# Optimization experiments

Measured on AMD Instinct MI355X. Metric: run time of the kernel, lower is better.

Reference implementation:

```python
import jax, jax.numpy as jnp
import numpy as np

N, NB, H, D = 192, 3, 8, 10
HU, HE = [16, 8], [4, 2]
Ne = N * N


def setup_inputs() -> dict:
    key = jax.random.key(0)
    ks = jax.random.split(key, 20)
    g = lambda i, s: jax.random.normal(ks[i], s, jnp.float32)
    xav = lambda i, s: g(i, s) * 0.1  # small-scale init standing in for xavier
    return {
        "X": g(0, (N, D)),
        "A": g(1, (NB, N, N)),
        "E": g(2, (NB, N, N)),
        "e2n_adj": g(3, (N, Ne)),
        # node-path params, stacked over [attr, head]
        "w_n0": xav(4, (NB, H, D, HU[0])), "b_n0": jnp.zeros((NB, H, HU[0])),
        "as0": xav(5, (NB, H, HU[0])), "an0": xav(6, (NB, H, HU[0])),
        "w_n1": xav(7, (NB, H, H * HU[0], HU[1])), "b_n1": jnp.zeros((NB, H, HU[1])),
        "as1": xav(8, (NB, H, HU[1])), "an1": xav(9, (NB, H, HU[1])),
        # edge-to-node params, stacked over [head] (shared across attrs)
        "w_e0": xav(10, (H, NB, HE[0])), "b_e0": jnp.zeros((H, HE[0])),
        "w_ct0": xav(11, (H, HU[0] + HE[0], HU[0])), "b_ct0": jnp.zeros((H, HU[0])),
        "aes0": xav(12, (H, HU[0])), "aen0": xav(13, (H, HE[0])),
        "w_e1": xav(14, (H, H * HE[0], HE[1])), "b_e1": jnp.zeros((H, HE[1])),
        "w_ct1": xav(15, (H, HU[1] + HE[1], HU[1])), "b_ct1": jnp.zeros((H, HU[1])),
        "aes1": xav(16, (H, HU[1])), "aen1": xav(17, (H, HE[1])),
    }


def reference(X, A, E, e2n_adj,
              w_n0, b_n0, as0, an0, w_n1, b_n1, as1, an1,
              w_e0, b_e0, w_ct0, b_ct0, aes0, aen0,
              w_e1, b_e1, w_ct1, b_ct1, aes1, aen1):
    # Eval mode: dropout is identity.
    lrelu = lambda x: jax.nn.leaky_relu(x, 0.2)
    nb = A.shape[0]
    n = X.shape[0]
    E_e2n = E.reshape(nb, -1).T  # [Ne, nb]; col attr == E[attr].flatten()
    node_p = [(w_n0, b_n0, as0, an0), (w_n1, b_n1, as1, an1)]
    edge_p = [(w_e0, b_e0, w_ct0, b_ct0, aes0, aen0),
              (w_e1, b_e1, w_ct1, b_ct1, aes1, aen1)]
    outs = []
    for attr in range(nb):
        A_attr = A[attr]
        h_list = [X]
        X_head, X_edge, E_info = X, E_e2n, E[attr]
        for hid in range(len(node_p)):
            wn, bn, asf, anf = (p[attr] for p in node_p[hid])
            we, be, wct, bct, aes, aen = edge_p[hid]
            feats = jnp.einsum('nd,hdf->hnf', X_head, wn)        # [H,N,F]
            fe = jnp.einsum('ed,hdf->hef', X_edge, we)           # [H,Ne,Fe]
            s = jnp.einsum('hnf,hf->hn', feats, aes)
            t = jnp.einsum('hef,hf->he', fe, aen)
            # edge-to-node attention: [H,N,Ne]
            att = jax.nn.softmax(lrelu(s[:, :, None] + t[:, None, :]) + e2n_adj[None], -1)
            nfe = jnp.einsum('hne,hef->hnf', att, fe) + be[:, None, :]
            f2 = jnp.einsum('hnd,hdf->hnf', jnp.concatenate([feats, nfe], -1), wct) + bct[:, None, :]
            s2 = jnp.einsum('hnf,hf->hn', f2, asf)
            t2 = jnp.einsum('hnf,hf->hn', f2, anf)
            d2 = jnp.einsum('hnm,mk->hnk', s2[:, :, None] + t2[:, None, :], E_info)
            att2 = jax.nn.softmax(lrelu(d2) + A_attr[None], -1)  # [H,N,N]
            nf = jax.nn.elu(jnp.einsum('hnm,hmf->hnf', att2, f2) + bn[:, None, :])
            h1 = jnp.transpose(nf, (1, 0, 2)).reshape(n, -1)     # head concat
            h_list.append(h1)
            X_head = h1
            X_edge = jnp.transpose(fe, (1, 0, 2)).reshape(fe.shape[1], -1)
            E_info = att2[-1]  # last head's post-softmax dense (as in torch)
        outs.append(jnp.concatenate(h_list, -1)[:, None, :])  # skip connection
    return jnp.concatenate(outs, 1)  # [N, nb_attribute, D + H*HU0 + H*HU1]
```

## Files before the change

kernel.cpp:

```cpp
#include <hip/hip_runtime.h>
#include <hip/hip_bf16.h>

#define NN 192
#define NBA 3
#define NH 8
#define ND 10
#define NE_ (NN*NN)
#define NE2 (NE_/2)
#define OUTC 202

typedef unsigned int u32;
typedef unsigned short u16;
typedef __attribute__((ext_vector_type(2))) _Float16 h2v;
typedef __attribute__((ext_vector_type(8))) _Float16 f16x8;
typedef __attribute__((ext_vector_type(4))) float f32x4;

static const size_t OFF_ET0P  = 0;
static const size_t OFF_ET50P = OFF_ET0P  + 147456;
static const size_t OFF_ET1P  = OFF_ET50P + 147456;
static const size_t OFF_ET51P = OFF_ET1P  + 147456;
static const size_t OFF_FT0P  = OFF_ET51P + 147456;
static const size_t OFF_FT1P  = OFF_FT0P  + 589824;
static const size_t OFF_EAP   = OFF_FT1P  + 294912;
static const size_t OFF_XH1   = OFF_EAP   + 3538944;
static const size_t OFF_EINF  = OFF_XH1   + 73728;
static const size_t OFF_ES0   = OFF_EINF  + 110592;
static const size_t OFF_ES50  = OFF_ES0   + 4608;
static const size_t OFF_ES1   = OFF_ES50  + 4608;
static const size_t OFF_ES51  = OFF_ES1   + 4608;
static const size_t OFF_WT1   = OFF_ES51  + 4608;
static const size_t OFF_PART  = OFF_WT1   + 3072;
static const size_t OFF_RED   = OFF_PART  + 1474560;
static const size_t OFF_F2    = OFF_RED   + 23040;
static const size_t OFF_S2    = OFF_F2    + 73728;
static const size_t OFF_T2    = OFF_S2    + 4608;
static const size_t OFF_TE    = OFF_T2    + 4608;
static const size_t OFF_CS    = OFF_TE    + 4608;

__device__ __forceinline__ u32 h2u(h2v h) { union { h2v h; u32 u; } c; c.h = h; return c.u; }
__device__ __forceinline__ h2v u2h(u32 u) { union { u32 u; h2v h; } c; c.u = u; return c.h; }
__device__ __forceinline__ u32 packh(float a, float b) {
    h2v h; h.x = (_Float16)a; h.y = (_Float16)b; return h2u(h);
}

__global__ __launch_bounds__(256) void k_pre(
    const float* __restrict__ E, const float* __restrict__ adj,
    const float* __restrict__ X,
    const float* __restrict__ we0, const float* __restrict__ aen0,
    const float* __restrict__ we1, const float* __restrict__ aen1,
    const float* __restrict__ wn0, const float* __restrict__ aes0,
    const float* __restrict__ wn1, const float* __restrict__ aes1,
    u32* __restrict__ et0P, u32* __restrict__ et50P,
    u32* __restrict__ et1P, u32* __restrict__ et51P,
    u32* __restrict__ ft0P, u32* __restrict__ ft1P,
    u32* __restrict__ eaP,
    u32* __restrict__ es0, u32* __restrict__ es50,
    float* __restrict__ wt1)
{
    int b = blockIdx.x, tid = threadIdx.x;
    if (b < 72) {
        __shared__ float w0s[96], a0s[32], w1s[512], a1s[16];
        for (int i = tid; i < 96;  i += 256) w0s[i] = we0[i];
        for (int i = tid; i < 32;  i += 256) a0s[i] = aen0[i];
        for (int i = tid; i < 512; i += 256) w1s[i] = we1[i];
        for (int i = tid; i < 16;  i += 256) a1s[i] = aen1[i];
        __syncthreads();
        int ep = b*256 + tid;
        int e0 = 2*ep;
        float2 E0 = *(const float2*)(E + e0);
        float2 E1 = *(const float2*)(E + NE_ + e0);
        float2 E2 = *(const float2*)(E + 2*NE_ + e0);
        float fa[32], fb[32];
        #pragma unroll
        for (int h = 0; h < 8; h++) {
            float ta = 0.f, tb = 0.f;
            #pragma unroll
            for (int f = 0; f < 4; f++) {
                float wa = w0s[h*12+f], wb = w0s[h*12+4+f], wc = w0s[h*12+8+f];
                float va = E0.x*wa + E1.x*wb + E2.x*wc;
                float vb = E0.y*wa + E1.y*wb + E2.y*wc;
                fa[h*4+f] = va; fb[h*4+f] = vb;
                ft0P[(size_t)(h*4+f)*NE2 + ep] = packh(va, vb);
                ta += va * a0s[h*4+f];
                tb += vb * a0s[h*4+f];
            }
            et0P [h*NE2 + ep] = packh(__expf(ta), __expf(tb));
            et50P[h*NE2 + ep] = packh(__expf(0.2f*ta), __expf(0.2f*tb));
        }
        #pragma unroll
        for (int h = 0; h < 8; h++) {
            float aa = 0.f, ba = 0.f, ab = 0.f, bb = 0.f;
            #pragma unroll
            for (int d = 0; d < 32; d++) {
                float w0 = w1s[(h*32+d)*2], w1 = w1s[(h*32+d)*2+1];
                aa += fa[d] * w0;  ba += fa[d] * w1;
                ab += fb[d] * w0;  bb += fb[d] * w1;
            }
            ft1P[(size_t)(h*2+0)*NE2 + ep] = packh(aa, ab);
            ft1P[(size_t)(h*2+1)*NE2 + ep] = packh(ba, bb);
            float ta = aa*a1s[h*2] + ba*a1s[h*2+1];
            float tb = ab*a1s[h*2] + bb*a1s[h*2+1];
            et1P [h*NE2 + ep] = packh(__expf(ta), __expf(tb));
            et51P[h*NE2 + ep] = packh(__expf(0.2f*ta), __expf(0.2f*tb));
        }
    } else if (b < 1800) {
        int idx = (b - 72)*256 + tid;
        int n = idx / 2304, c8 = idx % 2304;
        const float* ap = adj + (size_t)n*NE_ + c8*16;
        u32 o[8];
        #pragma unroll
        for (int q = 0; q < 4; q++) {
            float4 v = *(const float4*)(ap + q*4);
            o[2*q]   = packh(__expf(v.x), __expf(v.y));
            o[2*q+1] = packh(__expf(v.z), __expf(v.w));
        }
        u32* dst = eaP + (size_t)n*NE2 + c8*8;
        *(uint4*)(dst)     = make_uint4(o[0], o[1], o[2], o[3]);
        *(uint4*)(dst + 4) = make_uint4(o[4], o[5], o[6], o[7]);
    } else if (b == 1800) {
        for (int v = tid; v < 3072; v += 256) {
            int a = v >> 10, rem = v & 1023, h = rem >> 7, d = rem & 127;
            float w = 0.f;
            #pragma unroll
            for (int f = 0; f < 8; f++)
                w += wn1[(((size_t)a*NH + h)*128 + d)*8 + f] * aes1[h*8 + f];
            wt1[v] = w;
        }
    } else {
        int ah = b - 1801;
        int a = ah / NH, h = ah % NH;
        __shared__ float wt0[ND];
        if (tid < ND) {
            float w = 0.f;
            #pragma unroll
            for (int f = 0; f < 16; f++)
                w += wn0[(((size_t)a*NH + h)*ND + tid)*16 + f] * aes0[h*16 + f];
            wt0[tid] = w;
        }
        __syncthreads();
        if (tid < NN) {
            float s = 0.f;
            #pragma unroll
            for (int d = 0; d < ND; d++) s += X[tid*ND + d] * wt0[d];
            es0 [ah*NN + tid] = packh(__expf(s), __expf(s));
            es50[ah*NN + tid] = packh(__expf(0.2f*s), __expf(0.2f*s));
        }
    }
}

template<int FE>
__global__ __launch_bounds__(512, 3) void k_att3(
    const u32* __restrict__ es_,
    const u32* __restrict__ es5_,
    const u32* __restrict__ etP,
    const u32* __restrict__ et5P,
    const u32* __restrict__ feP,
    const u32* __restrict__ eaP,
    float* __restrict__ part)
{
    constexpr int S = 64, EPB = NE_/S, TILES = EPB/32;
    constexpr int EP2 = EPB/2;
    constexpr int ROWP = EP2 + 4;
    constexpr size_t PA = (size_t)S*12*NH*(FE+1)*16;
    __shared__ u32 sea[16*ROWP];

    int h = threadIdx.x >> 6, lane = threadIdx.x & 63;
    int fr = lane & 15, kg = lane >> 4;
    int split = blockIdx.x, ntile = blockIdx.y;
    int nm = ntile*16 + fr;
    int p0 = split*EP2;

    {
        int r = threadIdx.x >> 5, c0 = threadIdx.x & 31;
        const u32* src = eaP + (size_t)(ntile*16 + r)*NE2 + p0;
        #pragma unroll
        for (int i = 0; i < 9; i++)
            sea[r*ROWP + c0 + i*32] = src[c0 + i*32];
    }

    h2v esh[NBA], es5h[NBA];
    #pragma unroll
    for (int a = 0; a < NBA; a++) {
        esh[a]  = u2h(es_ [(a*NH + h)*NN + nm]);
        es5h[a] = u2h(es5_[(a*NH + h)*NN + nm]);
    }

    const u32* etp  = etP  + (size_t)h*NE2 + p0 + kg*4;
    const u32* et5p = et5P + (size_t)h*NE2 + p0 + kg*4;
    const u32* fp   = feP  + ((size_t)h*FE + (fr < FE ? fr : 0))*NE2 + p0 + kg*4;
    u32 bfill = (fr == FE) ? 0x3C003C00u : 0u;
    uint4 bc = make_uint4(bfill, bfill, bfill, bfill);

    f32x4 acc[NBA];
    #pragma unroll
    for (int a = 0; a < NBA; a++) acc[a] = (f32x4){0.f, 0.f, 0.f, 0.f};

    __syncthreads();

    const u32* seap = sea + fr*ROWP + kg*4;
    #pragma unroll 2
    for (int t = 0; t < TILES; t++) {
        uint4 etq  = *(const uint4*)(etp  + t*16);
        uint4 et5q = *(const uint4*)(et5p + t*16);
        uint4 eaq  = *(const uint4*)(seap + t*16);
        uint4 bq = bc;
        if (fr < FE) bq = *(const uint4*)(fp + t*16);
        union { uint4 u; f16x8 v; } B; B.u = bq;

        u32 etw[4]  = {etq.x,  etq.y,  etq.z,  etq.w};
        u32 et5w[4] = {et5q.x, et5q.y, et5q.z, et5q.w};
        u32 eaw[4]  = {eaq.x,  eaq.y,  eaq.z,  eaq.w};
        h2v g1[4], g2[4];
        #pragma unroll
        for (int p = 0; p < 4; p++) {
            h2v ea = u2h(eaw[p]);
            g1[p] = u2h(etw[p])  * ea;
            g2[p] = u2h(et5w[p]) * ea;
        }
        #pragma unroll
        for (int a = 0; a < NBA; a++) {
            union { uint4 u; f16x8 v; } A;
            u32 aw[4];
            #pragma unroll
            for (int p = 0; p < 4; p++) {
                h2v wv = __builtin_elementwise_max(esh[a] * g1[p], es5h[a] * g2[p]);
                aw[p] = h2u(wv);
            }
            A.u = make_uint4(aw[0], aw[1], aw[2], aw[3]);
            acc[a] = __builtin_amdgcn_mfma_f32_16x16x32_f16(A.v, B.v, acc[a], 0, 0, 0);
        }
    }

    if (fr <= FE) {
        float* pp = part + ((((size_t)split*12 + ntile)*NH + h)*(FE+1) + fr)*16 + kg*4;
        #pragma unroll
        for (int a = 0; a < NBA; a++)
            *(f32x4*)(pp + (size_t)a*PA) = acc[a];
    }
}

template<int FE>
__global__ __launch_bounds__(256) void k_red(
    const float* __restrict__ part, float* __restrict__ red)
{
    constexpr int S = 64, W = (FE+1)*16;
    constexpr size_t SSTR = (size_t)12*NH*W;
    constexpr size_t PA = (size_t)S*SSTR;
    int nt = blockIdx.x >> 3, h = blockIdx.x & 7;
    int t = threadIdx.x;
    if (t >= NBA*W) return;
    int a = t / W, i = t % W;
    const float* pp = part + (size_t)a*PA + ((size_t)nt*NH + h)*W + i;
    float v = 0.f;
    #pragma unroll 8
    for (int s = 0; s < S; s++) v += pp[(size_t)s*SSTR];
    red[((size_t)a*96 + nt*8 + h)*W + i] = v;
}

template<int DIN, int F, int FE>
__global__ __launch_bounds__(256) void k_mid(
    const float* __restrict__ Xh, int xstride,
    const float* __restrict__ wn,
    const float* __restrict__ be,
    const float* __restrict__ wct,
    const float* __restrict__ bct,
    const float* __restrict__ asf,
    const float* __restrict__ anf,
    const float* __restrict__ red,
    float* __restrict__ f2, float* __restrict__ s2, float* __restrict__ t2)
{
    constexpr int DCT = F + FE, W = (FE+1)*16;
    int n = blockIdx.x, attr = blockIdx.y;
    int h = threadIdx.x >> 5, lane = threadIdx.x & 31;
    const float* Xp = Xh + (size_t)attr*xstride;
    const float* wnp = wn + (size_t)attr*NH*DIN*F;
    float* f2p = f2 + (size_t)attr*NH*NN*16;
    float v = 0.f;
    if (lane <= FE)
        v = red[((size_t)attr*96 + (n>>4)*8 + h)*W + lane*16 + (n & 15)];
    float den = __shfl(v, FE, 32);
    float nfe = (lane < FE) ? v/den + be[h*FE+lane] : 0.f;
    float fv = 0.f;
    if (lane < F) {
        for (int d = 0; d < DIN; d++) fv += Xp[n*DIN+d] * wnp[(h*DIN+d)*F+lane];
    }
    __shared__ float c[NH][DCT];
    if (lane < F)  c[h][lane]     = fv;
    if (lane < FE) c[h][F + lane] = nfe;
    __syncthreads();
    float f2v = 0.f;
    if (lane < F) {
        f2v = bct[h*F+lane];
        #pragma unroll
        for (int d = 0; d < DCT; d++) f2v += c[h][d] * wct[(h*DCT+d)*F+lane];
        f2p[((size_t)h*NN + n)*16 + lane] = f2v;
    }
    float s2p = (lane < F) ? f2v * asf[attr*NH*F + h*F+lane] : 0.f;
    float t2p = (lane < F) ? f2v * anf[attr*NH*F + h*F+lane] : 0.f;
    #pragma unroll
    for (int m = 1; m < 32; m <<= 1) { s2p += __shfl_xor(s2p, m); t2p += __shfl_xor(t2p, m); }
    if (lane == 0) { s2[attr*NH*NN + h*NN+n] = s2p; t2[attr*NH*NN + h*NN+n] = t2p; }
}

__global__ __launch_bounds__(192) void k_te(
    const float* __restrict__ Einfo, size_t estride,
    const float* __restrict__ t2,
    float* __restrict__ tE, float* __restrict__ cs)
{
    int h = blockIdx.x, attr = blockIdx.y, k = threadIdx.x;
    const float* Ep = Einfo + (size_t)attr*estride;
    float a = 0.f, c = 0.f;
    for (int m = 0; m < NN; m++) {
        float ev = Ep[m*NN + k];
        a += t2[attr*NH*NN + h*NN + m] * ev;
        c += ev;
    }
    tE[attr*NH*NN + h*NN + k] = a;
    if (h == 0) cs[attr*NN + k] = c;
}

template<int F, int LAYER>
__global__ __launch_bounds__(256) void k_out(
    const float* __restrict__ A,
    const float* __restrict__ s2, const float* __restrict__ tE,
    const float* __restrict__ cs, const float* __restrict__ f2,
    const float* __restrict__ bn,
    const float* __restrict__ X,
    float* __restrict__ out,
    float* __restrict__ xh1, float* __restrict__ einfo,
    const float* __restrict__ wt1,
    u32* __restrict__ es1, u32* __restrict__ es51)
{
    int n = blockIdx.x, attr = blockIdx.y;
    int h = threadIdx.x >> 5, lane = threadIdx.x & 31;
    const float* Aattr = A + (size_t)attr*NE_;
    const float* f2p = f2 + (size_t)attr*NH*NN*16;
    float s2h = s2[attr*NH*NN + h*NN + n];
    float z[6];
    #pragma unroll
    for (int c6 = 0; c6 < 6; c6++) {
        int k = lane + 32*c6;
        float d2v = s2h * cs[attr*NN + k] + tE[attr*NH*NN + h*NN + k];
        z[c6] = fmaxf(d2v, 0.2f*d2v) + Aattr[n*NN + k];
    }
    float mx = z[0];
    #pragma unroll
    for (int c6 = 1; c6 < 6; c6++) mx = fmaxf(mx, z[c6]);
    #pragma unroll
    for (int m = 1; m < 32; m <<= 1) mx = fmaxf(mx, __shfl_xor(mx, m));
    float w[6], den = 0.f;
    #pragma unroll
    for (int c6 = 0; c6 < 6; c6++) { w[c6] = __expf(z[c6] - mx); den += w[c6]; }
    #pragma unroll
    for (int m = 1; m < 32; m <<= 1) den += __shfl_xor(den, m);
    __shared__ float attL[NH][NN];
    __shared__ float xrow[128];
    #pragma unroll
    for (int c6 = 0; c6 < 6; c6++) attL[h][lane + 32*c6] = w[c6];
    __syncthreads();
    float r = 0.f;
    if (lane < F) {
        for (int k = 0; k < NN; k++) r += attL[h][k] * f2p[((size_t)h*NN + k)*16 + lane];
        r = r/den + bn[attr*NH*F + h*F + lane];
        r = r > 0.f ? r : __expf(r) - 1.f;
        out[((size_t)n*NBA + attr)*OUTC + (LAYER == 0 ? 10 : 138) + h*F + lane] = r;
        if (LAYER == 0) {
            xh1[(size_t)attr*NN*128 + n*128 + h*16 + lane] = r;
            xrow[h*16 + lane] = r;
        }
    }
    if (LAYER == 0 && h == 7) {
        #pragma unroll
        for (int c6 = 0; c6 < 6; c6++)
            einfo[(size_t)attr*NE_ + n*NN + lane + 32*c6] = w[c6] / den;
    }
    if (LAYER == 0 && h == 0 && lane < ND)
        out[((size_t)n*NBA + attr)*OUTC + lane] = X[n*ND + lane];
    if (LAYER == 0) {
        __syncthreads();
        float sp = 0.f;
        const float* wp = wt1 + ((size_t)attr*NH + h)*128;
        #pragma unroll
        for (int q = 0; q < 4; q++) sp += xrow[lane*4+q] * wp[lane*4+q];
        #pragma unroll
        for (int m = 1; m < 32; m <<= 1) sp += __shfl_xor(sp, m);
        if (lane == 0) {
            es1 [(attr*NH + h)*NN + n] = packh(__expf(sp), __expf(sp));
            es51[(attr*NH + h)*NN + n] = packh(__expf(0.2f*sp), __expf(0.2f*sp));
        }
    }
}

extern "C" void kernel_launch(void* const* d_in, const int* in_sizes, int n_in,
                              void* d_out, int out_size, void* d_ws, size_t ws_size,
                              hipStream_t stream) {
    const float* X    = (const float*)d_in[0];
    const float* A    = (const float*)d_in[1];
    const float* E    = (const float*)d_in[2];
    const float* adj  = (const float*)d_in[3];
    const float* w_n0 = (const float*)d_in[4];
    const float* b_n0 = (const float*)d_in[5];
    const float* as0  = (const float*)d_in[6];
    const float* an0  = (const float*)d_in[7];
    const float* w_n1 = (const float*)d_in[8];
    const float* b_n1 = (const float*)d_in[9];
    const float* as1  = (const float*)d_in[10];
    const float* an1  = (const float*)d_in[11];
    const float* w_e0 = (const float*)d_in[12];
    const float* b_e0 = (const float*)d_in[13];
    const float* w_ct0= (const float*)d_in[14];
    const float* b_ct0= (const float*)d_in[15];
    const float* aes0 = (const float*)d_in[16];
    const float* aen0 = (const float*)d_in[17];
    const float* w_e1 = (const float*)d_in[18];
    const float* b_e1 = (const float*)d_in[19];
    const float* w_ct1= (const float*)d_in[20];
    const float* b_ct1= (const float*)d_in[21];
    const float* aes1 = (const float*)d_in[22];
    const float* aen1 = (const float*)d_in[23];

    float* w      = (float*)d_ws;
    u32* et0P  = (u32*)(w + OFF_ET0P);
    u32* et50P = (u32*)(w + OFF_ET50P);
    u32* et1P  = (u32*)(w + OFF_ET1P);
    u32* et51P = (u32*)(w + OFF_ET51P);
    u32* ft0P  = (u32*)(w + OFF_FT0P);
    u32* ft1P  = (u32*)(w + OFF_FT1P);
    u32* eaP   = (u32*)(w + OFF_EAP);
    float* xh1   = w + OFF_XH1;
    float* einfo = w + OFF_EINF;
    u32* es0   = (u32*)(w + OFF_ES0);
    u32* es50  = (u32*)(w + OFF_ES50);
    u32* es1   = (u32*)(w + OFF_ES1);
    u32* es51  = (u32*)(w + OFF_ES51);
    float* wt1   = w + OFF_WT1;
    float* part  = w + OFF_PART;
    float* red   = w + OFF_RED;
    float* f2    = w + OFF_F2;
    float* s2    = w + OFF_S2;
    float* t2    = w + OFF_T2;
    float* tE    = w + OFF_TE;
    float* cs    = w + OFF_CS;
    float* out   = (float*)d_out;

    k_pre<<<dim3(1825), dim3(256), 0, stream>>>(
        E, adj, X, w_e0, aen0, w_e1, aen1, w_n0, aes0, w_n1, aes1,
        et0P, et50P, et1P, et51P, ft0P, ft1P, eaP, es0, es50, wt1);

    k_att3<4><<<dim3(64,12), dim3(512), 0, stream>>>(
        es0, es50, et0P, et50P, ft0P, eaP, part);
    k_red<4><<<dim3(96), dim3(256), 0, stream>>>(part, red);
    k_mid<10,16,4><<<dim3(NN,NBA), dim3(256), 0, stream>>>(
        X, 0, w_n0, b_e0, w_ct0, b_ct0, as0, an0, red, f2, s2, t2);
    k_te<<<dim3(8,NBA), dim3(192), 0, stream>>>(E, (size_t)NE_, t2, tE, cs);
    k_out<16,0><<<dim3(NN,NBA), dim3(256), 0, stream>>>(
        A, s2, tE, cs, f2, b_n0, X, out, xh1, einfo, wt1, es1, es51);

    k_att3<2><<<dim3(64,12), dim3(512), 0, stream>>>(
        es1, es51, et1P, et51P, ft1P, eaP, part);
    k_red<2><<<dim3(96), dim3(256), 0, stream>>>(part, red);
    k_mid<128,8,2><<<dim3(NN,NBA), dim3(256), 0, stream>>>(
        xh1, NN*128, w_n1, b_e1, w_ct1, b_ct1, as1, an1, red, f2, s2, t2);
    k_te<<<dim3(8,NBA), dim3(192), 0, stream>>>(einfo, (size_t)NE_, t2, tE, cs);
    k_out<8,1><<<dim3(NN,NBA), dim3(256), 0, stream>>>(
        A, s2, tE, cs, f2, b_n1, X, out, xh1, einfo, wt1, es1, es51);
}
```

Baseline: 110.7 us.

## Interleave edge exp tables and transpose f2 for vectorized aggregation

The two per-head edge exponential tables (exp(t) and exp(0.2t)) are interleaved into one buffer in 4-word groups, so the attention kernel fetches both from adjacent addresses instead of two separate streams. The f2 features are stored transposed (feature-major over nodes), so the output kernel's weighted sum can use float4 loads from contiguous rows rather than strided scalar loads. An unroll pragma is also added to the k_te loop. Together these aim to cut memory transactions and improve coalescing, at the cost of more complex indexing in producer and consumer.

```diff
diff --git a/kernel.cpp b/kernel.cpp
--- a/kernel.cpp
+++ b/kernel.cpp
@@ -15,11 +15,9 @@
 typedef __attribute__((ext_vector_type(8))) _Float16 f16x8;
 typedef __attribute__((ext_vector_type(4))) float f32x4;
 
-static const size_t OFF_ET0P  = 0;
-static const size_t OFF_ET50P = OFF_ET0P  + 147456;
-static const size_t OFF_ET1P  = OFF_ET50P + 147456;
-static const size_t OFF_ET51P = OFF_ET1P  + 147456;
-static const size_t OFF_FT0P  = OFF_ET51P + 147456;
+static const size_t OFF_ETI0  = 0;
+static const size_t OFF_ETI1  = OFF_ETI0  + 294912;
+static const size_t OFF_FT0P  = OFF_ETI1  + 294912;
 static const size_t OFF_FT1P  = OFF_FT0P  + 589824;
 static const size_t OFF_EAP   = OFF_FT1P  + 294912;
 static const size_t OFF_XH1   = OFF_EAP   + 3538944;
@@ -50,8 +48,7 @@
     const float* __restrict__ we1, const float* __restrict__ aen1,
     const float* __restrict__ wn0, const float* __restrict__ aes0,
     const float* __restrict__ wn1, const float* __restrict__ aes1,
-    u32* __restrict__ et0P, u32* __restrict__ et50P,
-    u32* __restrict__ et1P, u32* __restrict__ et51P,
+    u32* __restrict__ etI0, u32* __restrict__ etI1,
     u32* __restrict__ ft0P, u32* __restrict__ ft1P,
     u32* __restrict__ eaP,
     u32* __restrict__ es0, u32* __restrict__ es50,
@@ -66,6 +63,7 @@
         for (int i = tid; i < 16;  i += 256) a1s[i] = aen1[i];
         __syncthreads();
         int ep = b*256 + tid;
+        int gslot = ((ep >> 2) << 3) + (ep & 3);
         int e0 = 2*ep;
         float2 E0 = *(const float2*)(E + e0);
         float2 E1 = *(const float2*)(E + NE_ + e0);
@@ -84,8 +82,8 @@
                 ta += va * a0s[h*4+f];
                 tb += vb * a0s[h*4+f];
             }
-            et0P [h*NE2 + ep] = packh(__expf(ta), __expf(tb));
-            et50P[h*NE2 + ep] = packh(__expf(0.2f*ta), __expf(0.2f*tb));
+            etI0[(size_t)h*2*NE2 + gslot]     = packh(__expf(ta), __expf(tb));
+            etI0[(size_t)h*2*NE2 + gslot + 4] = packh(__expf(0.2f*ta), __expf(0.2f*tb));
         }
         #pragma unroll
         for (int h = 0; h < 8; h++) {
@@ -100,8 +98,8 @@
             ft1P[(size_t)(h*2+1)*NE2 + ep] = packh(ba, bb);
             float ta = aa*a1s[h*2] + ba*a1s[h*2+1];
             float tb = ab*a1s[h*2] + bb*a1s[h*2+1];
-            et1P [h*NE2 + ep] = packh(__expf(ta), __expf(tb));
-            et51P[h*NE2 + ep] = packh(__expf(0.2f*ta), __expf(0.2f*tb));
+            etI1[(size_t)h*2*NE2 + gslot]     = packh(__expf(ta), __expf(tb));
+            etI1[(size_t)h*2*NE2 + gslot + 4] = packh(__expf(0.2f*ta), __expf(0.2f*tb));
         }
     } else if (b < 1800) {
         int idx = (b - 72)*256 + tid;
@@ -152,8 +150,7 @@
 __global__ __launch_bounds__(512, 3) void k_att3(
     const u32* __restrict__ es_,
     const u32* __restrict__ es5_,
-    const u32* __restrict__ etP,
-    const u32* __restrict__ et5P,
+    const u32* __restrict__ etI,
     const u32* __restrict__ feP,
     const u32* __restrict__ eaP,
     float* __restrict__ part)
@@ -185,9 +182,8 @@
         es5h[a] = u2h(es5_[(a*NH + h)*NN + nm]);
     }
 
-    const u32* etp  = etP  + (size_t)h*NE2 + p0 + kg*4;
-    const u32* et5p = et5P + (size_t)h*NE2 + p0 + kg*4;
-    const u32* fp   = feP  + ((size_t)h*FE + (fr < FE ? fr : 0))*NE2 + p0 + kg*4;
+    const u32* etg = etI + (size_t)h*2*NE2 + ((size_t)split*72 + kg)*8;
+    const u32* fp  = feP + ((size_t)h*FE + (fr < FE ? fr : 0))*NE2 + p0 + kg*4;
     u32 bfill = (fr == FE) ? 0x3C003C00u : 0u;
     uint4 bc = make_uint4(bfill, bfill, bfill, bfill);
 
@@ -200,8 +196,8 @@
     const u32* seap = sea + fr*ROWP + kg*4;
     #pragma unroll 2
     for (int t = 0; t < TILES; t++) {
-        uint4 etq  = *(const uint4*)(etp  + t*16);
-        uint4 et5q = *(const uint4*)(et5p + t*16);
+        uint4 etq  = *(const uint4*)(etg + t*32);
+        uint4 et5q = *(const uint4*)(etg + t*32 + 4);
         uint4 eaq  = *(const uint4*)(seap + t*16);
         uint4 bq = bc;
         if (fr < FE) bq = *(const uint4*)(fp + t*16);
@@ -267,14 +263,14 @@
     const float* __restrict__ asf,
     const float* __restrict__ anf,
     const float* __restrict__ red,
-    float* __restrict__ f2, float* __restrict__ s2, float* __restrict__ t2)
+    float* __restrict__ f2T,
+    float* __restrict__ s2, float* __restrict__ t2)
 {
     constexpr int DCT = F + FE, W = (FE+1)*16;
     int n = blockIdx.x, attr = blockIdx.y;
     int h = threadIdx.x >> 5, lane = threadIdx.x & 31;
     const float* Xp = Xh + (size_t)attr*xstride;
     const float* wnp = wn + (size_t)attr*NH*DIN*F;
-    float* f2p = f2 + (size_t)attr*NH*NN*16;
     float v = 0.f;
     if (lane <= FE)
         v = red[((size_t)attr*96 + (n>>4)*8 + h)*W + lane*16 + (n & 15)];
@@ -293,7 +289,7 @@
         f2v = bct[h*F+lane];
         #pragma unroll
         for (int d = 0; d < DCT; d++) f2v += c[h][d] * wct[(h*DCT+d)*F+lane];
-        f2p[((size_t)h*NN + n)*16 + lane] = f2v;
+        f2T[(size_t)attr*NH*F*NN + (size_t)(h*F+lane)*NN + n] = f2v;
     }
     float s2p = (lane < F) ? f2v * asf[attr*NH*F + h*F+lane] : 0.f;
     float t2p = (lane < F) ? f2v * anf[attr*NH*F + h*F+lane] : 0.f;
@@ -310,6 +306,7 @@
     int h = blockIdx.x, attr = blockIdx.y, k = threadIdx.x;
     const float* Ep = Einfo + (size_t)attr*estride;
     float a = 0.f, c = 0.f;
+    #pragma unroll 4
     for (int m = 0; m < NN; m++) {
         float ev = Ep[m*NN + k];
         a += t2[attr*NH*NN + h*NN + m] * ev;
@@ -323,7 +320,7 @@
 __global__ __launch_bounds__(256) void k_out(
     const float* __restrict__ A,
     const float* __restrict__ s2, const float* __restrict__ tE,
-    const float* __restrict__ cs, const float* __restrict__ f2,
+    const float* __restrict__ cs, const float* __restrict__ f2T,
     const float* __restrict__ bn,
     const float* __restrict__ X,
     float* __restrict__ out,
@@ -334,7 +331,6 @@
     int n = blockIdx.x, attr = blockIdx.y;
     int h = threadIdx.x >> 5, lane = threadIdx.x & 31;
     const float* Aattr = A + (size_t)attr*NE_;
-    const float* f2p = f2 + (size_t)attr*NH*NN*16;
     float s2h = s2[attr*NH*NN + h*NN + n];
     float z[6];
     #pragma unroll
@@ -360,7 +356,13 @@
     __syncthreads();
     float r = 0.f;
     if (lane < F) {
-        for (int k = 0; k < NN; k++) r += attL[h][k] * f2p[((size_t)h*NN + k)*16 + lane];
+        const float* frow = f2T + (size_t)attr*NH*F*NN + (size_t)(h*F+lane)*NN;
+        #pragma unroll 4
+        for (int k4 = 0; k4 < NN/4; k4++) {
+            float4 aq = *(const float4*)(&attL[h][k4*4]);
+            float4 fq = *(const float4*)(frow + k4*4);
+            r += aq.x*fq.x + aq.y*fq.y + aq.z*fq.z + aq.w*fq.w;
+        }
         r = r/den + bn[attr*NH*F + h*F + lane];
         r = r > 0.f ? r : __expf(r) - 1.f;
         out[((size_t)n*NBA + attr)*OUTC + (LAYER == 0 ? 10 : 138) + h*F + lane] = r;
@@ -420,10 +422,8 @@
     const float* aen1 = (const float*)d_in[23];
 
     float* w      = (float*)d_ws;
-    u32* et0P  = (u32*)(w + OFF_ET0P);
-    u32* et50P = (u32*)(w + OFF_ET50P);
-    u32* et1P  = (u32*)(w + OFF_ET1P);
-    u32* et51P = (u32*)(w + OFF_ET51P);
+    u32* etI0  = (u32*)(w + OFF_ETI0);
+    u32* etI1  = (u32*)(w + OFF_ETI1);
     u32* ft0P  = (u32*)(w + OFF_FT0P);
     u32* ft1P  = (u32*)(w + OFF_FT1P);
     u32* eaP   = (u32*)(w + OFF_EAP);
@@ -436,7 +436,7 @@
     float* wt1   = w + OFF_WT1;
     float* part  = w + OFF_PART;
     float* red   = w + OFF_RED;
-    float* f2    = w + OFF_F2;
+    float* f2T   = w + OFF_F2;
     float* s2    = w + OFF_S2;
     float* t2    = w + OFF_T2;
     float* tE    = w + OFF_TE;
@@ -445,23 +445,23 @@
 
     k_pre<<<dim3(1825), dim3(256), 0, stream>>>(
         E, adj, X, w_e0, aen0, w_e1, aen1, w_n0, aes0, w_n1, aes1,
-        et0P, et50P, et1P, et51P, ft0P, ft1P, eaP, es0, es50, wt1);
+        etI0, etI1, ft0P, ft1P, eaP, es0, es50, wt1);
 
     k_att3<4><<<dim3(64,12), dim3(512), 0, stream>>>(
-        es0, es50, et0P, et50P, ft0P, eaP, part);
+        es0, es50, etI0, ft0P, eaP, part);
     k_red<4><<<dim3(96), dim3(256), 0, stream>>>(part, red);
     k_mid<10,16,4><<<dim3(NN,NBA), dim3(256), 0, stream>>>(
-        X, 0, w_n0, b_e0, w_ct0, b_ct0, as0, an0, red, f2, s2, t2);
+        X, 0, w_n0, b_e0, w_ct0, b_ct0, as0, an0, red, f2T, s2, t2);
     k_te<<<dim3(8,NBA), dim3(192), 0, stream>>>(E, (size_t)NE_, t2, tE, cs);
     k_out<16,0><<<dim3(NN,NBA), dim3(256), 0, stream>>>(
-        A, s2, tE, cs, f2, b_n0, X, out, xh1, einfo, wt1, es1, es51);
+        A, s2, tE, cs, f2T, b_n0, X, out, xh1, einfo, wt1, es1, es51);
 
     k_att3<2><<<dim3(64,12), dim3(512), 0, stream>>>(
-        es1, es51, et1P, et51P, ft1P, eaP, part);
+        es1, es51, etI1, ft1P, eaP, part);
     k_red<2><<<dim3(96), dim3(256), 0, stream>>>(part, red);
     k_mid<128,8,2><<<dim3(NN,NBA), dim3(256), 0, stream>>>(
-        xh1, NN*128, w_n1, b_e1, w_ct1, b_ct1, as1, an1, red, f2, s2, t2);
+        xh1, NN*128, w_n1, b_e1, w_ct1, b_ct1, as1, an1, red, f2T, s2, t2);
     k_te<<<dim3(8,NBA), dim3(192), 0, stream>>>(einfo, (size_t)NE_, t2, tE, cs);
     k_out<8,1><<<dim3(NN,NBA), dim3(256), 0, stream>>>(
-        A, s2, tE, cs, f2, b_n1, X, out, xh1, einfo, wt1, es1, es51);
-}
+        A, s2, tE, cs, f2T, b_n1, X, out, xh1, einfo, wt1, es1, es51);
+}
```

After: 126.5 us. +14.3%, slower.
